# Kernel tuning notes

Measured on AMD Instinct MI355X. Metric: run time of the kernel, lower is better.

The kernel has to match this reference:

```python
import jax, jax.numpy as jnp
import numpy as np

B, T, F, H, O = 256, 512, 128, 256, 1


def setup_inputs() -> dict:
    key = jax.random.key(0)
    ks = jax.random.split(key, 32)
    def rn(i, shape, s=0.05):
        return jax.random.normal(ks[i], shape, jnp.float32) * s
    inp = {
        "x": jax.random.normal(ks[0], (B, T, F), jnp.float32),
        # BatchNorm1d (eval mode) params / running stats
        "bn_gamma": 1.0 + rn(1, (F,), 0.1),
        "bn_beta": rn(2, (F,), 0.1),
        "bn_mean": rn(3, (F,), 0.1),
        "bn_var": 1.0 + jax.random.uniform(ks[4], (F,), jnp.float32) * 0.5,
        # SpatialAttention linear F->F
        "sa_W": rn(5, (F, F)), "sa_b": rn(6, (F,)),
        # layer_in F->H
        "in_W": rn(7, (H, F)), "in_b": rn(8, (H,)),
        # LSTM layer 0 (input H) and layer 1 (input H), torch gate order i,f,g,o
        "Wih0": rn(9, (4 * H, H)), "Whh0": rn(10, (4 * H, H)),
        "bih0": rn(11, (4 * H,)), "bhh0": rn(12, (4 * H,)),
        "Wih1": rn(13, (4 * H, H)), "Whh1": rn(14, (4 * H, H)),
        "bih1": rn(15, (4 * H,)), "bhh1": rn(16, (4 * H,)),
        # TemporalAttention: hidden_to_input H->F, T_A F->F
        "ta_hW": rn(17, (F, H)), "ta_hb": rn(18, (F,)),
        "ta_W": rn(19, (F, F)), "ta_b": rn(20, (F,)),
        # layer_out F->O, no bias
        "out_W": rn(21, (O, F)),
    }
    return inp


def _lstm_layer(seq, Wih, Whh, bih, bhh):
    # seq: [T, B, H_in]
    Hd = Whh.shape[1]
    b = bih + bhh
    def step(carry, xt):
        h, c = carry
        g = xt @ Wih.T + h @ Whh.T + b  # [B, 4H]
        i, f, gg, o = jnp.split(g, 4, axis=-1)
        c = jax.nn.sigmoid(f) * c + jax.nn.sigmoid(i) * jnp.tanh(gg)
        h = jax.nn.sigmoid(o) * jnp.tanh(c)
        return (h, c), h
    nb = seq.shape[1]
    init = (jnp.zeros((nb, Hd), seq.dtype), jnp.zeros((nb, Hd), seq.dtype))
    _, hs = jax.lax.scan(step, init, seq)
    return hs  # [T, B, H]


def reference(x, bn_gamma, bn_beta, bn_mean, bn_var, sa_W, sa_b, in_W, in_b,
              Wih0, Whh0, bih0, bhh0, Wih1, Whh1, bih1, bhh1,
              ta_hW, ta_hb, ta_W, ta_b, out_W):
    # BatchNorm1d (eval): normalize per feature
    xb = (x - bn_mean) * jax.lax.rsqrt(bn_var + 1e-5) * bn_gamma + bn_beta
    # Spatial attention (vectorized over all timesteps at once)
    alpha = jax.nn.softmax(jax.nn.sigmoid(xb @ sa_W.T + sa_b), axis=-1)
    xs = xb * alpha
    # layer_in (dropout is identity in eval mode)
    h = xs @ in_W.T + in_b  # [B, T, H]
    seq = jnp.swapaxes(h, 0, 1)  # [T, B, H]
    seq = _lstm_layer(seq, Wih0, Whh0, bih0, bhh0)
    seq = _lstm_layer(seq, Wih1, Whh1, bih1, bhh1)
    h_t = jnp.swapaxes(seq, 0, 1)  # [B, T, H]
    # Temporal attention
    total = h_t @ ta_hW.T + ta_hb  # [B, T, F]
    beta = jax.nn.softmax(jax.nn.relu(total @ ta_W.T + ta_b), axis=1)
    ctx = jnp.sum(beta * total, axis=1)  # [B, F]
    out = (ctx @ out_W.T).squeeze()  # [B]
    return out
```

## Files before the change

### kernel.cpp

```cpp
#include <hip/hip_runtime.h>

typedef __attribute__((ext_vector_type(8))) short short8;
typedef __attribute__((ext_vector_type(4))) float floatx4;
typedef __attribute__((ext_vector_type(2))) unsigned long long ull2;

__device__ __forceinline__ unsigned short f2bf(float f) {
  unsigned int u = __float_as_uint(f);
  unsigned int lsb = (u >> 16) & 1u;
  u += 0x7fffu + lsb;
  return (unsigned short)(u >> 16);
}
__device__ __forceinline__ float bf2f(unsigned short u) {
  unsigned int x = ((unsigned int)u) << 16;
  return __uint_as_float(x);
}
__device__ __forceinline__ float sigm(float x) { return 1.f / (1.f + __expf(-x)); }
__device__ __forceinline__ float tanh_fast(float x) { return 2.f / (1.f + __expf(-2.f * x)) - 1.f; }
__device__ __forceinline__ floatx4 mfma16(short8 a, short8 b, floatx4 c) {
  return __builtin_amdgcn_mfma_f32_16x16x32_bf16(a, b, c, 0, 0, 0);
}

__global__ void wc_kernel(const float* __restrict__ Wih0, const float* __restrict__ inW,
                          const float* __restrict__ inb, const float* __restrict__ bih0,
                          const float* __restrict__ bhh0, unsigned short* __restrict__ Wc,
                          float* __restrict__ bc) {
  const int n = blockIdx.x;
  const int k = threadIdx.x;
  float a = 0.f;
  for (int j = 0; j < 256; ++j) a += Wih0[n * 256 + j] * inW[j * 128 + k];
  Wc[n * 128 + k] = f2bf(a);
  if (k == 0) {
    float bsum = bih0[n] + bhh0[n];
    for (int j = 0; j < 256; ++j) bsum += Wih0[n * 256 + j] * inb[j];
    bc[n] = bsum;
  }
}

__global__ void cvt_kernel(unsigned short* __restrict__ dst, const float* __restrict__ src, int n) {
  int i = blockIdx.x * 256 + threadIdx.x;
  if (i < n) dst[i] = f2bf(src[i]);
}

__global__ void addb_kernel(float* __restrict__ b1, const float* __restrict__ xa,
                            const float* __restrict__ ya, int n) {
  int i = blockIdx.x * 256 + threadIdx.x;
  if (i < n) b1[i] = xa[i] + ya[i];
}

__global__ __launch_bounds__(128) void bnsa_kernel(
    const float* __restrict__ x, const float* __restrict__ gamma,
    const float* __restrict__ beta, const float* __restrict__ mean,
    const float* __restrict__ var, const float* __restrict__ saW,
    const float* __restrict__ sab, unsigned short* __restrict__ xs, int rowsPerWg) {
  __shared__ unsigned short saT[128 * 128];
  __shared__ float xbuf[128];
  __shared__ float ebuf[128];
  const int j = threadIdx.x;
  for (int k = 0; k < 128; ++k) saT[k * 128 + j] = f2bf(saW[j * 128 + k]);
  const float g = gamma[j], bt = beta[j], mn = mean[j];
  const float istd = rsqrtf(var[j] + 1e-5f);
  const float sb = sab[j];
  __syncthreads();
  const long row0 = (long)blockIdx.x * rowsPerWg;
  for (int it = 0; it < rowsPerWg; ++it) {
    const long row = row0 + it;
    const float xv = x[row * 128 + j];
    const float xb = (xv - mn) * istd * g + bt;
    xbuf[j] = xb;
    __syncthreads();
    float s = sb;
#pragma unroll 8
    for (int k = 0; k < 128; ++k) s += xbuf[k] * bf2f(saT[k * 128 + j]);
    const float e = __expf(sigm(s));
    ebuf[j] = e;
    __syncthreads();
    float sum = 0.f;
#pragma unroll 8
    for (int k = 0; k < 128; ++k) sum += ebuf[k];
    xs[row * 128 + j] = f2bf(xb * (e / sum));
    __syncthreads();
  }
}

__global__ __launch_bounds__(512, 2) void persist_kernel(
    const unsigned short* __restrict__ xs,
    const unsigned short* __restrict__ Wc, const float* __restrict__ bc,
    const unsigned short* __restrict__ Whh0,
    const unsigned short* __restrict__ Wih1, const float* __restrict__ b1,
    const unsigned short* __restrict__ Whh1,
    const unsigned short* __restrict__ tahWg, const float* __restrict__ tahb,
    const unsigned short* __restrict__ taWg, const float* __restrict__ tab,
    const float* __restrict__ outW,
    ull2* __restrict__ ex,
    float* __restrict__ out) {
  __shared__ unsigned short tahWs[128 * 264];
  __shared__ unsigned short taWs[128 * 136];
  __shared__ unsigned short h0buf[16 * 264];
  __shared__ unsigned short h1buf[16 * 264];
  __shared__ float gatebuf[2][8 * 16 * 20];
  __shared__ unsigned short totB[16 * 136];

  const int tid = threadIdx.x;
  const int wv = tid >> 6, lane = tid & 63;
  const int lm = lane & 15, q = lane >> 4;
  const int slice = blockIdx.x >> 4, group = blockIdx.x & 15;
  const int g = wv & 3, ht = wv >> 2;
  const int b0 = group * 16;
  const int hcol = slice * 32 + ht * 16 + lm;
  const int ng = g * 256 + hcol;
  const int fcol = wv * 16 + lm;

  for (int i = tid; i < 128 * 256; i += 512) tahWs[(i >> 8) * 264 + (i & 255)] = tahWg[i];
  for (int i = tid; i < 128 * 128; i += 512) taWs[(i >> 7) * 136 + (i & 127)] = taWg[i];
  for (int i = tid; i < 16 * 264; i += 512) { h0buf[i] = 0; h1buf[i] = 0; }

  short8 Wcf[4], W0f[8], W1if[8], W1hf[8];
#pragma unroll
  for (int kt = 0; kt < 4; ++kt) Wcf[kt] = *(const short8*)&Wc[(size_t)ng * 128 + kt * 32 + q * 8];
#pragma unroll
  for (int kt = 0; kt < 8; ++kt) {
    W0f[kt] = *(const short8*)&Whh0[(size_t)ng * 256 + kt * 32 + q * 8];
    W1if[kt] = *(const short8*)&Wih1[(size_t)ng * 256 + kt * 32 + q * 8];
    W1hf[kt] = *(const short8*)&Whh1[(size_t)ng * 256 + kt * 32 + q * 8];
  }
  const float bcv = bc[ng], b1v = b1[ng];
  const float tahbv = tahb[fcol], tabv = tab[fcol], outWv = outW[fcol];

  floatx4 cst0 = (floatx4){0.f, 0.f, 0.f, 0.f};
  floatx4 cst1 = (floatx4){0.f, 0.f, 0.f, 0.f};
  float num[4] = {0.f, 0.f, 0.f, 0.f}, den[4] = {0.f, 0.f, 0.f, 0.f};

  const unsigned short* xrow = xs + (size_t)(b0 + lm) * 65536 + q * 8;
  short8 axf[4], axn[4];
#pragma unroll
  for (int kt = 0; kt < 4; ++kt) axf[kt] = *(const short8*)(xrow + kt * 32);

  const int ew = ((slice >> 1) << 8) + (((slice & 1) * 32 + ht * 16 + lm) << 2) + q;
  ull2* const exg = ex + (size_t)group * 2048;

  const int npidx = ((wv >> 2) << 1) | (wv & 1);
  const int nt = npidx * 64 + lane;
  unsigned voBase[8];
#pragma unroll
  for (int L = 0; L < 2; ++L)
#pragma unroll
    for (int j = 0; j < 4; ++j) voBase[L * 4 + j] = (unsigned)((L * 1024 + j * 256 + nt) << 4);
  const int cb = nt >> 2, qq = nt & 3;

  __syncthreads();

  for (int t = 0; t <= 512; ++t) {
    const int p = t & 1;
    const unsigned fvu = (unsigned)(t + 1);

    {
      floatx4 aW = (floatx4){0.f, 0.f, 0.f, 0.f};
      floatx4 aH = (floatx4){bcv, bcv, bcv, bcv};
#pragma unroll
      for (int kt = 0; kt < 4; ++kt) aW = mfma16(axf[kt], Wcf[kt], aW);
#pragma unroll
      for (int kt = 0; kt < 8; ++kt) {
        const short8 a = *(const short8*)&h0buf[lm * 264 + kt * 32 + q * 8];
        aH = mfma16(a, W0f[kt], aH);
      }
      const floatx4 acc = aW + aH;
#pragma unroll
      for (int r = 0; r < 4; ++r) gatebuf[0][(wv * 16 + q * 4 + r) * 20 + lm] = acc[r];
    }
    {
      const size_t tn = (t < 511) ? t + 1 : 511;
#pragma unroll
      for (int kt = 0; kt < 4; ++kt) axn[kt] = *(const short8*)(xrow + tn * 128 + kt * 32);
    }
    {
      floatx4 aI = (floatx4){b1v, b1v, b1v, b1v};
      floatx4 aH = (floatx4){0.f, 0.f, 0.f, 0.f};
#pragma unroll
      for (int kt = 0; kt < 8; ++kt) {
        const short8 a = *(const short8*)&h0buf[lm * 264 + kt * 32 + q * 8];
        aI = mfma16(a, W1if[kt], aI);
      }
#pragma unroll
      for (int kt = 0; kt < 8; ++kt) {
        const short8 a = *(const short8*)&h1buf[lm * 264 + kt * 32 + q * 8];
        aH = mfma16(a, W1hf[kt], aH);
      }
      const floatx4 acc = aI + aH;
#pragma unroll
      for (int r = 0; r < 4; ++r) gatebuf[1][(wv * 16 + q * 4 + r) * 20 + lm] = acc[r];
    }
    __syncthreads();

    if (g < 2) {
      const int L = g;
      unsigned short hb[4];
      if (L == 0) {
#pragma unroll
        for (int r = 0; r < 4; ++r) {
          const int m = q * 4 + r;
          const float iv = gatebuf[0][((ht * 4 + 0) * 16 + m) * 20 + lm];
          const float fv = gatebuf[0][((ht * 4 + 1) * 16 + m) * 20 + lm];
          const float gv = gatebuf[0][((ht * 4 + 2) * 16 + m) * 20 + lm];
          const float ov = gatebuf[0][((ht * 4 + 3) * 16 + m) * 20 + lm];
          const float cn = sigm(fv) * cst0[r] + sigm(iv) * tanh_fast(gv);
          cst0[r] = cn;
          hb[r] = f2bf(sigm(ov) * tanh_fast(cn));
        }
      } else {
#pragma unroll
        for (int r = 0; r < 4; ++r) hb[r] = 0;
        if (t > 0) {
#pragma unroll
          for (int r = 0; r < 4; ++r) {
            const int m = q * 4 + r;
            const float iv = gatebuf[1][((ht * 4 + 0) * 16 + m) * 20 + lm];
            const float fv = gatebuf[1][((ht * 4 + 1) * 16 + m) * 20 + lm];
            const float gv = gatebuf[1][((ht * 4 + 2) * 16 + m) * 20 + lm];
            const float ov = gatebuf[1][((ht * 4 + 3) * 16 + m) * 20 + lm];
            const float cn = sigm(fv) * cst1[r] + sigm(iv) * tanh_fast(gv);
            cst1[r] = cn;
            hb[r] = f2bf(sigm(ov) * tanh_fast(cn));
          }
        }
      }
      const unsigned long long sq = (unsigned long long)fvu << 32;
      const unsigned long long qlo = (unsigned long long)hb[0] | ((unsigned long long)hb[1] << 16) | sq;
      const unsigned long long qhi = (unsigned long long)hb[2] | ((unsigned long long)hb[3] << 16) | sq;
      unsigned long long* wp =
          (unsigned long long*)(exg + (size_t)p * 32768 + (size_t)L * 1024 + ew);
      __hip_atomic_store(&wp[0], qlo, __ATOMIC_RELAXED, __HIP_MEMORY_SCOPE_AGENT);
      __hip_atomic_store(&wp[1], qhi, __ATOMIC_RELAXED, __HIP_MEMORY_SCOPE_AGENT);
    }

    floatx4 ta;
    if (t >= 2) {
      ta = (floatx4){tahbv, tahbv, tahbv, tahbv};
#pragma unroll
      for (int kt = 0; kt < 8; ++kt) {
        const short8 a = *(const short8*)&h1buf[lm * 264 + kt * 32 + q * 8];
        ta = mfma16(a, *(const short8*)&tahWs[fcol * 264 + kt * 32 + q * 8], ta);
      }
#pragma unroll
      for (int r = 0; r < 4; ++r) totB[(q * 4 + r) * 136 + fcol] = f2bf(ta[r]);
    }
    __syncthreads();
    if (t >= 2) {
      floatx4 sa = (floatx4){tabv, tabv, tabv, tabv};
#pragma unroll
      for (int kt = 0; kt < 4; ++kt) {
        const short8 a = *(const short8*)&totB[lm * 136 + kt * 32 + q * 8];
        sa = mfma16(a, *(const short8*)&taWs[fcol * 136 + kt * 32 + q * 8], sa);
      }
#pragma unroll
      for (int r = 0; r < 4; ++r) {
        const float e = __expf(fmaxf(sa[r], 0.f));
        num[r] += e * ta[r];
        den[r] += e;
      }
    }

    if (g >= 2) {
      const unsigned pterm = (unsigned)p << 19;
      const unsigned v0o = voBase[0] + pterm, v1o = voBase[1] + pterm;
      const unsigned v2o = voBase[2] + pterm, v3o = voBase[3] + pterm;
      const unsigned v4o = voBase[4] + pterm, v5o = voBase[5] + pterm;
      const unsigned v6o = voBase[6] + pterm, v7o = voBase[7] + pterm;
      ull2 d0, d1, d2, d3, e0, e1, e2, e3;
      unsigned bad;
      do {
        asm volatile(
            "global_load_dwordx4 %0, %8, %16 sc0 sc1\n\t"
            "global_load_dwordx4 %1, %9, %16 sc0 sc1\n\t"
            "global_load_dwordx4 %2, %10, %16 sc0 sc1\n\t"
            "global_load_dwordx4 %3, %11, %16 sc0 sc1\n\t"
            "global_load_dwordx4 %4, %12, %16 sc0 sc1\n\t"
            "global_load_dwordx4 %5, %13, %16 sc0 sc1\n\t"
            "global_load_dwordx4 %6, %14, %16 sc0 sc1\n\t"
            "global_load_dwordx4 %7, %15, %16 sc0 sc1\n\t"
            "s_waitcnt vmcnt(0)"
            : "=&v"(d0), "=&v"(d1), "=&v"(d2), "=&v"(d3),
              "=&v"(e0), "=&v"(e1), "=&v"(e2), "=&v"(e3)
            : "v"(v0o), "v"(v1o), "v"(v2o), "v"(v3o),
              "v"(v4o), "v"(v5o), "v"(v6o), "v"(v7o),
              "s"(exg)
            : "memory");
        bad = ((unsigned)(d0.x >> 32) != fvu) | ((unsigned)(d0.y >> 32) != fvu) |
              ((unsigned)(d1.x >> 32) != fvu) | ((unsigned)(d1.y >> 32) != fvu) |
              ((unsigned)(d2.x >> 32) != fvu) | ((unsigned)(d2.y >> 32) != fvu) |
              ((unsigned)(d3.x >> 32) != fvu) | ((unsigned)(d3.y >> 32) != fvu) |
              ((unsigned)(e0.x >> 32) != fvu) | ((unsigned)(e0.y >> 32) != fvu) |
              ((unsigned)(e1.x >> 32) != fvu) | ((unsigned)(e1.y >> 32) != fvu) |
              ((unsigned)(e2.x >> 32) != fvu) | ((unsigned)(e2.y >> 32) != fvu) |
              ((unsigned)(e3.x >> 32) != fvu) | ((unsigned)(e3.y >> 32) != fvu);
      } while (bad);
      {
        const int c0 = cb, c1 = 64 + cb, c2 = 128 + cb, c3 = 192 + cb;
        h0buf[(qq * 4 + 0) * 264 + c0] = (unsigned short)d0.x;
        h0buf[(qq * 4 + 1) * 264 + c0] = (unsigned short)(d0.x >> 16);
        h0buf[(qq * 4 + 2) * 264 + c0] = (unsigned short)d0.y;
        h0buf[(qq * 4 + 3) * 264 + c0] = (unsigned short)(d0.y >> 16);
        h0buf[(qq * 4 + 0) * 264 + c1] = (unsigned short)d1.x;
        h0buf[(qq * 4 + 1) * 264 + c1] = (unsigned short)(d1.x >> 16);
        h0buf[(qq * 4 + 2) * 264 + c1] = (unsigned short)d1.y;
        h0buf[(qq * 4 + 3) * 264 + c1] = (unsigned short)(d1.y >> 16);
        h0buf[(qq * 4 + 0) * 264 + c2] = (unsigned short)d2.x;
        h0buf[(qq * 4 + 1) * 264 + c2] = (unsigned short)(d2.x >> 16);
        h0buf[(qq * 4 + 2) * 264 + c2] = (unsigned short)d2.y;
        h0buf[(qq * 4 + 3) * 264 + c2] = (unsigned short)(d2.y >> 16);
        h0buf[(qq * 4 + 0) * 264 + c3] = (unsigned short)d3.x;
        h0buf[(qq * 4 + 1) * 264 + c3] = (unsigned short)(d3.x >> 16);
        h0buf[(qq * 4 + 2) * 264 + c3] = (unsigned short)d3.y;
        h0buf[(qq * 4 + 3) * 264 + c3] = (unsigned short)(d3.y >> 16);
        h1buf[(qq * 4 + 0) * 264 + c0] = (unsigned short)e0.x;
        h1buf[(qq * 4 + 1) * 264 + c0] = (unsigned short)(e0.x >> 16);
        h1buf[(qq * 4 + 2) * 264 + c0] = (unsigned short)e0.y;
        h1buf[(qq * 4 + 3) * 264 + c0] = (unsigned short)(e0.y >> 16);
        h1buf[(qq * 4 + 0) * 264 + c1] = (unsigned short)e1.x;
        h1buf[(qq * 4 + 1) * 264 + c1] = (unsigned short)(e1.x >> 16);
        h1buf[(qq * 4 + 2) * 264 + c1] = (unsigned short)e1.y;
        h1buf[(qq * 4 + 3) * 264 + c1] = (unsigned short)(e1.y >> 16);
        h1buf[(qq * 4 + 0) * 264 + c2] = (unsigned short)e2.x;
        h1buf[(qq * 4 + 1) * 264 + c2] = (unsigned short)(e2.x >> 16);
        h1buf[(qq * 4 + 2) * 264 + c2] = (unsigned short)e2.y;
        h1buf[(qq * 4 + 3) * 264 + c2] = (unsigned short)(e2.y >> 16);
        h1buf[(qq * 4 + 0) * 264 + c3] = (unsigned short)e3.x;
        h1buf[(qq * 4 + 1) * 264 + c3] = (unsigned short)(e3.x >> 16);
        h1buf[(qq * 4 + 2) * 264 + c3] = (unsigned short)e3.y;
        h1buf[(qq * 4 + 3) * 264 + c3] = (unsigned short)(e3.y >> 16);
      }
    }
    __syncthreads();

#pragma unroll
    for (int kt = 0; kt < 4; ++kt) axf[kt] = axn[kt];
  }

  {
    floatx4 ta = (floatx4){tahbv, tahbv, tahbv, tahbv};
#pragma unroll
    for (int kt = 0; kt < 8; ++kt) {
      const short8 a = *(const short8*)&h1buf[lm * 264 + kt * 32 + q * 8];
      ta = mfma16(a, *(const short8*)&tahWs[fcol * 264 + kt * 32 + q * 8], ta);
    }
#pragma unroll
    for (int r = 0; r < 4; ++r) totB[(q * 4 + r) * 136 + fcol] = f2bf(ta[r]);
    __syncthreads();
    floatx4 sa = (floatx4){tabv, tabv, tabv, tabv};
#pragma unroll
    for (int kt = 0; kt < 4; ++kt) {
      const short8 a = *(const short8*)&totB[lm * 136 + kt * 32 + q * 8];
      sa = mfma16(a, *(const short8*)&taWs[fcol * 136 + kt * 32 + q * 8], sa);
    }
#pragma unroll
    for (int r = 0; r < 4; ++r) {
      const float e = __expf(fmaxf(sa[r], 0.f));
      num[r] += e * ta[r];
      den[r] += e;
    }
  }
  __syncthreads();

  float* red = &gatebuf[0][0];
#pragma unroll
  for (int r = 0; r < 4; ++r) red[(q * 4 + r) * 136 + fcol] = (num[r] / den[r]) * outWv;
  __syncthreads();
  if (slice == 0 && tid < 16) {
    float s = 0.f;
    for (int k = 0; k < 128; ++k) s += red[tid * 136 + k];
    out[b0 + tid] = s;
  }
}

extern "C" void kernel_launch(void* const* d_in, const int* in_sizes, int n_in,
                              void* d_out, int out_size, void* d_ws, size_t ws_size,
                              hipStream_t stream) {
  (void)in_sizes; (void)n_in; (void)out_size; (void)ws_size;
  const float* x    = (const float*)d_in[0];
  const float* bng  = (const float*)d_in[1];
  const float* bnb  = (const float*)d_in[2];
  const float* bnm  = (const float*)d_in[3];
  const float* bnv  = (const float*)d_in[4];
  const float* saW  = (const float*)d_in[5];
  const float* sab  = (const float*)d_in[6];
  const float* inW  = (const float*)d_in[7];
  const float* inb  = (const float*)d_in[8];
  const float* Wih0 = (const float*)d_in[9];
  const float* Whh0 = (const float*)d_in[10];
  const float* bih0 = (const float*)d_in[11];
  const float* bhh0 = (const float*)d_in[12];
  const float* Wih1 = (const float*)d_in[13];
  const float* Whh1 = (const float*)d_in[14];
  const float* bih1 = (const float*)d_in[15];
  const float* bhh1 = (const float*)d_in[16];
  const float* tahW = (const float*)d_in[17];
  const float* tahb = (const float*)d_in[18];
  const float* taW  = (const float*)d_in[19];
  const float* tab  = (const float*)d_in[20];
  const float* outW = (const float*)d_in[21];
  float* out = (float*)d_out;

  char* ws = (char*)d_ws;
  size_t off = 0;
  auto alloc = [&](size_t bytes) {
    char* p = ws + off;
    off += (bytes + 255) & ~(size_t)255;
    return p;
  };
  unsigned short* Wc    = (unsigned short*)alloc((size_t)1024 * 128 * 2);
  float* bc             = (float*)alloc(1024 * 4);
  float* b1             = (float*)alloc(1024 * 4);
  unsigned short* Whh0b = (unsigned short*)alloc((size_t)1024 * 256 * 2);
  unsigned short* Whh1b = (unsigned short*)alloc((size_t)1024 * 256 * 2);
  unsigned short* Wih1b = (unsigned short*)alloc((size_t)1024 * 256 * 2);
  unsigned short* tahWb = (unsigned short*)alloc((size_t)128 * 256 * 2);
  unsigned short* taWb  = (unsigned short*)alloc((size_t)128 * 128 * 2);
  unsigned short* xs    = (unsigned short*)alloc((size_t)131072 * 128 * 2);
  ull2* ex              = (ull2*)alloc((size_t)2 * 16 * 2 * 1024 * 16);

  hipLaunchKernelGGL(wc_kernel, dim3(1024), dim3(128), 0, stream, Wih0, inW, inb, bih0, bhh0, Wc, bc);
  hipLaunchKernelGGL(cvt_kernel, dim3(1024), dim3(256), 0, stream, Whh0b, Whh0, 262144);
  hipLaunchKernelGGL(cvt_kernel, dim3(1024), dim3(256), 0, stream, Whh1b, Whh1, 262144);
  hipLaunchKernelGGL(cvt_kernel, dim3(1024), dim3(256), 0, stream, Wih1b, Wih1, 262144);
  hipLaunchKernelGGL(cvt_kernel, dim3(128), dim3(256), 0, stream, tahWb, tahW, 32768);
  hipLaunchKernelGGL(cvt_kernel, dim3(64), dim3(256), 0, stream, taWb, taW, 16384);
  hipLaunchKernelGGL(addb_kernel, dim3(4), dim3(256), 0, stream, b1, bih1, bhh1, 1024);
  hipLaunchKernelGGL(bnsa_kernel, dim3(1024), dim3(128), 0, stream, x, bng, bnb, bnm, bnv, saW, sab, xs, 128);
  hipLaunchKernelGGL(persist_kernel, dim3(128), dim3(512), 0, stream, xs, Wc, bc, Whh0b, Wih1b,
                     b1, Whh1b, tahWb, tahb, taWb, tab, outW, ex, out);
}
```

Baseline: 2.354 ms.

## Use MFMA for batchnorm+spatial attention and merge weight prep kernels

```diff
diff --git a/kernel.cpp b/kernel.cpp
--- a/kernel.cpp
+++ b/kernel.cpp
@@ -20,66 +20,144 @@
   return __builtin_amdgcn_mfma_f32_16x16x32_bf16(a, b, c, 0, 0, 0);
 }
 
-__global__ void wc_kernel(const float* __restrict__ Wih0, const float* __restrict__ inW,
-                          const float* __restrict__ inb, const float* __restrict__ bih0,
-                          const float* __restrict__ bhh0, unsigned short* __restrict__ Wc,
-                          float* __restrict__ bc) {
-  const int n = blockIdx.x;
-  const int k = threadIdx.x;
-  float a = 0.f;
-  for (int j = 0; j < 256; ++j) a += Wih0[n * 256 + j] * inW[j * 128 + k];
-  Wc[n * 128 + k] = f2bf(a);
-  if (k == 0) {
-    float bsum = bih0[n] + bhh0[n];
-    for (int j = 0; j < 256; ++j) bsum += Wih0[n * 256 + j] * inb[j];
-    bc[n] = bsum;
-  }
-}
-
-__global__ void cvt_kernel(unsigned short* __restrict__ dst, const float* __restrict__ src, int n) {
-  int i = blockIdx.x * 256 + threadIdx.x;
-  if (i < n) dst[i] = f2bf(src[i]);
-}
-
-__global__ void addb_kernel(float* __restrict__ b1, const float* __restrict__ xa,
-                            const float* __restrict__ ya, int n) {
-  int i = blockIdx.x * 256 + threadIdx.x;
-  if (i < n) b1[i] = xa[i] + ya[i];
-}
-
-__global__ __launch_bounds__(128) void bnsa_kernel(
+__global__ __launch_bounds__(256) void prep_kernel(
+    const float* __restrict__ Wih0, const float* __restrict__ inW,
+    const float* __restrict__ inb, const float* __restrict__ bih0,
+    const float* __restrict__ bhh0, const float* __restrict__ Whh0,
+    const float* __restrict__ Whh1, const float* __restrict__ Wih1,
+    const float* __restrict__ tahW, const float* __restrict__ taW,
+    const float* __restrict__ bih1, const float* __restrict__ bhh1,
+    unsigned short* __restrict__ Wc, float* __restrict__ bc,
+    unsigned short* __restrict__ Whh0b, unsigned short* __restrict__ Whh1b,
+    unsigned short* __restrict__ Wih1b, unsigned short* __restrict__ tahWb,
+    unsigned short* __restrict__ taWb, float* __restrict__ b1) {
+  const int b = blockIdx.x, tid = threadIdx.x;
+  if (b < 512) {
+    const int n = b * 2 + (tid >> 7), k = tid & 127;
+    float a = 0.f;
+    for (int j = 0; j < 256; ++j) a += Wih0[n * 256 + j] * inW[j * 128 + k];
+    Wc[n * 128 + k] = f2bf(a);
+    if (k == 0) {
+      float bs = bih0[n] + bhh0[n];
+      for (int j = 0; j < 256; ++j) bs += Wih0[n * 256 + j] * inb[j];
+      bc[n] = bs;
+    }
+  } else if (b < 896) {
+    const int bb = b - 512;
+    const float* src = (bb < 128) ? Whh0 : (bb < 256) ? Whh1 : Wih1;
+    unsigned short* dst = (bb < 128) ? Whh0b : (bb < 256) ? Whh1b : Wih1b;
+    const int off = (bb & 127) * 2048 + tid * 8;
+    short8 v;
+#pragma unroll
+    for (int u = 0; u < 8; ++u) v[u] = (short)f2bf(src[off + u]);
+    *(short8*)&dst[off] = v;
+  } else if (b < 912) {
+    const int off = (b - 896) * 2048 + tid * 8;
+    short8 v;
+#pragma unroll
+    for (int u = 0; u < 8; ++u) v[u] = (short)f2bf(tahW[off + u]);
+    *(short8*)&tahWb[off] = v;
+  } else if (b < 920) {
+    const int off = (b - 912) * 2048 + tid * 8;
+    short8 v;
+#pragma unroll
+    for (int u = 0; u < 8; ++u) v[u] = (short)f2bf(taW[off + u]);
+    *(short8*)&taWb[off] = v;
+  } else {
+#pragma unroll
+    for (int u = 0; u < 4; ++u) {
+      const int i = tid * 4 + u;
+      b1[i] = bih1[i] + bhh1[i];
+    }
+  }
+}
+
+__global__ __launch_bounds__(256) void bnsa_kernel(
     const float* __restrict__ x, const float* __restrict__ gamma,
     const float* __restrict__ beta, const float* __restrict__ mean,
     const float* __restrict__ var, const float* __restrict__ saW,
-    const float* __restrict__ sab, unsigned short* __restrict__ xs, int rowsPerWg) {
-  __shared__ unsigned short saT[128 * 128];
-  __shared__ float xbuf[128];
-  __shared__ float ebuf[128];
-  const int j = threadIdx.x;
-  for (int k = 0; k < 128; ++k) saT[k * 128 + j] = f2bf(saW[j * 128 + k]);
-  const float g = gamma[j], bt = beta[j], mn = mean[j];
-  const float istd = rsqrtf(var[j] + 1e-5f);
-  const float sb = sab[j];
+    const float* __restrict__ sab, unsigned short* __restrict__ xs) {
+  __shared__ unsigned short saWs[128 * 132];
+  __shared__ unsigned short xbb[128 * 136];
+  const int tid = threadIdx.x;
+  const int wv = tid >> 6, lane = tid & 63;
+  const int lm = lane & 15, q = lane >> 4;
+  const long r0 = (long)blockIdx.x * 128;
+
+  for (int i = tid; i < 16384; i += 256) saWs[(i >> 7) * 132 + (i & 127)] = f2bf(saW[i]);
+  {
+    const int k0 = tid & 127;
+    const float mn = mean[k0];
+    const float is = rsqrtf(var[k0] + 1e-5f) * gamma[k0];
+    const float bt = beta[k0];
+    for (int i = tid; i < 16384; i += 256) {
+      const int m = i >> 7;
+      xbb[m * 136 + k0] = f2bf((x[(r0 + m) * 128 + k0] - mn) * is + bt);
+    }
+  }
   __syncthreads();
-  const long row0 = (long)blockIdx.x * rowsPerWg;
-  for (int it = 0; it < rowsPerWg; ++it) {
-    const long row = row0 + it;
-    const float xv = x[row * 128 + j];
-    const float xb = (xv - mn) * istd * g + bt;
-    xbuf[j] = xb;
-    __syncthreads();
-    float s = sb;
-#pragma unroll 8
-    for (int k = 0; k < 128; ++k) s += xbuf[k] * bf2f(saT[k * 128 + j]);
-    const float e = __expf(sigm(s));
-    ebuf[j] = e;
-    __syncthreads();
-    float sum = 0.f;
-#pragma unroll 8
-    for (int k = 0; k < 128; ++k) sum += ebuf[k];
-    xs[row * 128 + j] = f2bf(xb * (e / sum));
-    __syncthreads();
-  }
+
+  short8 af[2][4];
+#pragma unroll
+  for (int mt = 0; mt < 2; ++mt)
+#pragma unroll
+    for (int kt = 0; kt < 4; ++kt)
+      af[mt][kt] = *(const short8*)&xbb[(wv * 32 + mt * 16 + lm) * 136 + kt * 32 + q * 8];
+
+  floatx4 acc[2][8];
+#pragma unroll
+  for (int nt = 0; nt < 8; ++nt) {
+    const float sb = sab[nt * 16 + lm];
+    short8 bf[4];
+#pragma unroll
+    for (int kt = 0; kt < 4; ++kt)
+      bf[kt] = *(const short8*)&saWs[(nt * 16 + lm) * 132 + kt * 32 + q * 8];
+#pragma unroll
+    for (int mt = 0; mt < 2; ++mt) {
+      floatx4 a = (floatx4){sb, sb, sb, sb};
+#pragma unroll
+      for (int kt = 0; kt < 4; ++kt) a = mfma16(af[mt][kt], bf[kt], a);
+      acc[mt][nt] = a;
+    }
+  }
+  float tot[2][4];
+#pragma unroll
+  for (int mt = 0; mt < 2; ++mt)
+#pragma unroll
+    for (int r = 0; r < 4; ++r) {
+      float p = 0.f;
+#pragma unroll
+      for (int nt = 0; nt < 8; ++nt) {
+        const float e = __expf(sigm(acc[mt][nt][r]));
+        acc[mt][nt][r] = e;
+        p += e;
+      }
+      p += __shfl_xor(p, 1);
+      p += __shfl_xor(p, 2);
+      p += __shfl_xor(p, 4);
+      p += __shfl_xor(p, 8);
+      tot[mt][r] = p;
+    }
+  __syncthreads();
+  unsigned short* stg = saWs;
+#pragma unroll
+  for (int nt = 0; nt < 8; ++nt) {
+    const int col = nt * 16 + lm;
+    const float mn = mean[col];
+    const float is = rsqrtf(var[col] + 1e-5f) * gamma[col];
+    const float bt = beta[col];
+#pragma unroll
+    for (int mt = 0; mt < 2; ++mt)
+#pragma unroll
+      for (int r = 0; r < 4; ++r) {
+        const int row = wv * 32 + mt * 16 + q * 4 + r;
+        const float xb = (x[(r0 + row) * 128 + col] - mn) * is + bt;
+        stg[row * 128 + col] = f2bf(xb * (acc[mt][nt][r] / tot[mt][r]));
+      }
+  }
+  __syncthreads();
+  for (int i = tid * 8; i < 16384; i += 2048)
+    *(short8*)&xs[r0 * 128 + i] = *(const short8*)&stg[i];
 }
 
 __global__ __launch_bounds__(512, 2) void persist_kernel(
@@ -417,14 +495,11 @@
   unsigned short* xs    = (unsigned short*)alloc((size_t)131072 * 128 * 2);
   ull2* ex              = (ull2*)alloc((size_t)2 * 16 * 2 * 1024 * 16);
 
-  hipLaunchKernelGGL(wc_kernel, dim3(1024), dim3(128), 0, stream, Wih0, inW, inb, bih0, bhh0, Wc, bc);
-  hipLaunchKernelGGL(cvt_kernel, dim3(1024), dim3(256), 0, stream, Whh0b, Whh0, 262144);
-  hipLaunchKernelGGL(cvt_kernel, dim3(1024), dim3(256), 0, stream, Whh1b, Whh1, 262144);
-  hipLaunchKernelGGL(cvt_kernel, dim3(1024), dim3(256), 0, stream, Wih1b, Wih1, 262144);
-  hipLaunchKernelGGL(cvt_kernel, dim3(128), dim3(256), 0, stream, tahWb, tahW, 32768);
-  hipLaunchKernelGGL(cvt_kernel, dim3(64), dim3(256), 0, stream, taWb, taW, 16384);
-  hipLaunchKernelGGL(addb_kernel, dim3(4), dim3(256), 0, stream, b1, bih1, bhh1, 1024);
-  hipLaunchKernelGGL(bnsa_kernel, dim3(1024), dim3(128), 0, stream, x, bng, bnb, bnm, bnv, saW, sab, xs, 128);
+  hipLaunchKernelGGL(prep_kernel, dim3(921), dim3(256), 0, stream, Wih0, inW, inb, bih0, bhh0,
+                     Whh0, Whh1, Wih1, tahW, taW, bih1, bhh1, Wc, bc, Whh0b, Whh1b, Wih1b,
+                     tahWb, taWb, b1);
+  hipLaunchKernelGGL(bnsa_kernel, dim3(1024), dim3(256), 0, stream, x, bng, bnb, bnm, bnv, saW,
+                     sab, xs);
   hipLaunchKernelGGL(persist_kernel, dim3(128), dim3(512), 0, stream, xs, Wc, bc, Whh0b, Wih1b,
                      b1, Whh1b, tahWb, tahb, taWb, tab, outW, ex, out);
 }
```

Result: faster. 2.001 ms (-15.0%).
